# Kernel tuning notes

Measured on AMD Instinct MI355X. Metric: run time of the kernel, lower is better.

The kernel has to match this reference:

```python
import jax, jax.numpy as jnp
import numpy as np

D, H, COND, MLP_RATIO = 1024, 16, 1024, 4
HD = D // H
DFF = MLP_RATIO * D


def layer_norm(x, w, eps=1e-5):
    xf = x.astype(jnp.float32)
    mu = jnp.mean(xf, axis=-1, keepdims=True)
    var = jnp.mean((xf - mu) ** 2, axis=-1, keepdims=True)
    return (xf - mu) * jax.lax.rsqrt(var + eps) * w


def rms_norm(x, w, eps=1e-6):
    xf = x.astype(jnp.float32)
    rms = jnp.sqrt(jnp.mean(xf * xf, axis=-1, keepdims=True) + eps)
    return (xf / rms * w).astype(x.dtype)


def rotate_half(x):
    x1, x2 = x[..., : x.shape[-1] // 2], x[..., x.shape[-1] // 2:]
    return jnp.concatenate([-x2, x1], axis=-1)


def apply_rope(x, cos, sin):
    return x * cos + rotate_half(x) * sin


def setup_inputs() -> dict:
    key = jax.random.key(0)
    ks = jax.random.split(key, 16)
    B, S = 4, 2048
    pos = jnp.arange(S, dtype=jnp.float32)
    inv = 1.0 / (10000.0 ** (jnp.arange(0, HD, 2, dtype=jnp.float32) / HD))
    freqs = pos[:, None] * inv[None, :]              # (S, HD/2)
    emb = jnp.concatenate([freqs, freqs], axis=-1)   # (S, HD)
    return {
        "x": jax.random.normal(ks[0], (B, S, D), jnp.float32),
        "cos": jnp.cos(emb)[None, :, None, :],        # (1,S,1,HD)
        "sin": jnp.sin(emb)[None, :, None, :],
        "c": jax.random.normal(ks[1], (B, COND), jnp.float32),
        "norm1_w": jnp.ones((D,), jnp.float32),
        "Wqkv": jax.random.normal(ks[2], (D, 3 * D), jnp.float32) * 0.02,
        "Wout": jax.random.normal(ks[3], (D, D), jnp.float32) * 0.02,
        "q_norm_w": jnp.ones((HD,), jnp.float32),
        "k_norm_w": jnp.ones((HD,), jnp.float32),
        "norm2_w": jnp.ones((D,), jnp.float32),
        "W1": jax.random.normal(ks[4], (D, DFF), jnp.float32) * 0.02,
        "b1": jnp.zeros((DFF,), jnp.float32),
        "W2": jax.random.normal(ks[5], (DFF, D), jnp.float32) * 0.02,
        "b2": jnp.zeros((D,), jnp.float32),
        "ada_W": jax.random.normal(ks[6], (COND, 6 * D), jnp.float32) * 0.02,
        "ada_b": jnp.zeros((6 * D,), jnp.float32),
    }


def reference(x, cos, sin, c, norm1_w, Wqkv, Wout, q_norm_w, k_norm_w,
              norm2_w, W1, b1, W2, b2, ada_W, ada_b):
    B, S, _ = x.shape
    mod = (c @ ada_W + ada_b)[:, None, :]            # (B,1,6D)
    sh_msa, sc_msa, g_msa, sh_mlp, sc_mlp, g_mlp = jnp.split(mod, 6, axis=-1)

    x_norm = layer_norm(x, norm1_w) * (1 + sc_msa) + sh_msa
    qkv = (x_norm @ Wqkv).reshape(B, S, 3, H, HD)
    q, k, v = qkv[:, :, 0], qkv[:, :, 1], qkv[:, :, 2]  # (B,S,H,HD)
    q = apply_rope(rms_norm(q, q_norm_w), cos, sin)
    k = apply_rope(rms_norm(k, k_norm_w), cos, sin)

    scale = 1.0 / jnp.sqrt(jnp.float32(HD))
    logits = jnp.einsum('bqhd,bkhd->bhqk', q, k) * scale
    probs = jax.nn.softmax(logits, axis=-1)
    attn = jnp.einsum('bhqk,bkhd->bqhd', probs, v).reshape(B, S, D)

    x = x + g_msa * (attn @ Wout)

    x_norm = layer_norm(x, norm2_w) * (1 + sc_mlp) + sh_mlp
    h = jax.nn.gelu(x_norm @ W1 + b1, approximate=True)
    x = x + g_mlp * (h @ W2 + b2)
    return x
```

## Files before the change

kernel.cpp:

```cpp
#include <hip/hip_runtime.h>
#include <hip/hip_bf16.h>
#include <math.h>

typedef __bf16 bf16;
typedef __bf16 bf16x8 __attribute__((ext_vector_type(8)));
typedef __bf16 bf16x4 __attribute__((ext_vector_type(4)));
typedef float f32x4 __attribute__((ext_vector_type(4)));

#define S_LEN 2048
#define NTOK 8192
#define DIM 1024
#define NH 16
#define HEADD 64
#define DFF 4096
#define MODD 6144

__device__ __forceinline__ void gload_lds16(const bf16* g, bf16* l) {
  __builtin_amdgcn_global_load_lds(
      (const __attribute__((address_space(1))) void*)g,
      (__attribute__((address_space(3))) void*)l, 16, 0, 0);
}

__device__ __forceinline__ float gelu_tanh(float x) {
  float inner = 0.7978845608028654f * (x + 0.044715f * x * x * x);
  return 0.5f * x * (1.0f + tanhf(inner));
}

__global__ __launch_bounds__(256) void init_mod_kernel(
    const float* __restrict__ ada_b, float* __restrict__ mod) {
  int i = blockIdx.x * 256 + threadIdx.x;
  mod[i] = ada_b[i % MODD];
}

__global__ __launch_bounds__(256) void ada_gemm_kernel(
    const float* __restrict__ cnd, const float* __restrict__ W,
    float* __restrict__ mod) {
  int n = blockIdx.x * 256 + threadIdx.x;
  int k0 = blockIdx.y * 128;
  float a0 = 0.f, a1 = 0.f, a2 = 0.f, a3 = 0.f;
  for (int k = k0; k < k0 + 128; ++k) {
    float w = W[(size_t)k * MODD + n];
    a0 = fmaf(cnd[k], w, a0);
    a1 = fmaf(cnd[1024 + k], w, a1);
    a2 = fmaf(cnd[2048 + k], w, a2);
    a3 = fmaf(cnd[3072 + k], w, a3);
  }
  atomicAdd(&mod[n], a0);
  atomicAdd(&mod[MODD + n], a1);
  atomicAdd(&mod[2 * MODD + n], a2);
  atomicAdd(&mod[3 * MODD + n], a3);
}

__global__ __launch_bounds__(256) void transpose_cast_kernel(
    const float* __restrict__ W, bf16* __restrict__ Wt, int K, int N) {
  __shared__ float tile[32][33];
  int n0 = blockIdx.x * 32, k0 = blockIdx.y * 32;
  int r = threadIdx.x >> 3;
  int c4 = (threadIdx.x & 7) * 4;
  float4 v = *(const float4*)&W[(size_t)(k0 + r) * N + n0 + c4];
  tile[r][c4 + 0] = v.x; tile[r][c4 + 1] = v.y;
  tile[r][c4 + 2] = v.z; tile[r][c4 + 3] = v.w;
  __syncthreads();
  bf16x4 o;
  o[0] = (bf16)tile[c4 + 0][r];
  o[1] = (bf16)tile[c4 + 1][r];
  o[2] = (bf16)tile[c4 + 2][r];
  o[3] = (bf16)tile[c4 + 3][r];
  *(bf16x4*)&Wt[(size_t)(n0 + r) * K + k0 + c4] = o;
}

__global__ __launch_bounds__(256) void vtrans_kernel(
    const bf16* __restrict__ qkv, bf16* __restrict__ VT) {
  __shared__ __align__(16) bf16 t[64][72];
  const int bh = blockIdx.y;
  const int b = bh >> 4, h = bh & 15;
  const int s0 = blockIdx.x * 64;
  const int tid = threadIdx.x;
  {
    const int r = tid >> 2;
    const int c = (tid & 3) * 16;
    const bf16* src =
        qkv + (size_t)(b * S_LEN + s0 + r) * 3072 + 2048 + h * 64 + c;
    *(bf16x8*)&t[r][c] = *(const bf16x8*)src;
    *(bf16x8*)&t[r][c + 8] = *(const bf16x8*)(src + 8);
  }
  __syncthreads();
  {
    const int d = tid & 63;
    const int sc = (tid >> 6) * 16;
    bf16x8 o0, o1;
#pragma unroll
    for (int j = 0; j < 8; ++j) o0[j] = t[sc + j][d];
#pragma unroll
    for (int j = 0; j < 8; ++j) o1[j] = t[sc + 8 + j][d];
    bf16* dst = VT + (size_t)(bh * 64 + d) * S_LEN + s0 + sc;
    *(bf16x8*)dst = o0;
    *(bf16x8*)(dst + 8) = o1;
  }
}

__global__ __launch_bounds__(256) void ln_mod_kernel(
    const float* __restrict__ x, const float* __restrict__ w,
    const float* __restrict__ mod, int sh_off, int sc_off,
    bf16* __restrict__ out) {
  __shared__ float red[8];
  const int row = blockIdx.x;
  const int b = row >> 11;
  const int tid = threadIdx.x;
  const float4 v = ((const float4*)(x + (size_t)row * DIM))[tid];
  float s1 = v.x + v.y + v.z + v.w;
  float s2 = v.x * v.x + v.y * v.y + v.z * v.z + v.w * v.w;
  for (int off = 32; off > 0; off >>= 1) {
    s1 += __shfl_down(s1, off, 64);
    s2 += __shfl_down(s2, off, 64);
  }
  const int wid = tid >> 6;
  if ((tid & 63) == 0) { red[wid] = s1; red[4 + wid] = s2; }
  __syncthreads();
  s1 = red[0] + red[1] + red[2] + red[3];
  s2 = red[4] + red[5] + red[6] + red[7];
  const float mu = s1 * (1.0f / DIM);
  const float inv = rsqrtf(s2 * (1.0f / DIM) - mu * mu + 1e-5f);
  const int c = tid * 4;
  const float* mb = mod + (size_t)b * MODD;
  float xs[4] = {v.x, v.y, v.z, v.w};
  bf16x4 o;
#pragma unroll
  for (int j = 0; j < 4; ++j)
    o[j] = (bf16)(((xs[j] - mu) * inv) * w[c + j] * (1.0f + mb[sc_off + c + j]) +
                  mb[sh_off + c + j]);
  *(bf16x4*)(out + (size_t)row * DIM + c) = o;
}

template <int EPI>
__global__ __launch_bounds__(256) void gemm_bt(
    const bf16* __restrict__ A, const bf16* __restrict__ Bt,
    bf16* __restrict__ Cb, float* __restrict__ Cf,
    const float* __restrict__ bias, const float* __restrict__ gmod,
    const float* __restrict__ resid, int M, int N, int K) {
  __shared__ __align__(16) bf16 As[2][128 * 32];
  __shared__ __align__(16) bf16 Bs[2][128 * 32];
  const int tid = threadIdx.x;
  const int wid = tid >> 6;
  const int lane = tid & 63;
  const int l15 = lane & 15;
  const int quad = lane >> 4;
  const int m0 = blockIdx.y * 128;
  const int n0 = blockIdx.x * 128;
  const int wm = (wid & 1) * 64;
  const int wn = (wid >> 1) * 64;

  const int r0 = tid >> 2;
  const int cc0 = (tid & 3) * 8;
  const size_t a_base = (size_t)(m0 + r0) * K + cc0;
  const size_t a_base2 = (size_t)(m0 + 64 + r0) * K + cc0;
  const size_t b_base = (size_t)(n0 + r0) * K + cc0;
  const size_t b_base2 = (size_t)(n0 + 64 + r0) * K + cc0;

  f32x4 acc[4][4] = {};

  for (int kt = 0; kt < K; kt += 64) {
    gload_lds16(A + a_base + kt, &As[0][tid * 8]);
    gload_lds16(A + a_base2 + kt, &As[0][(256 + tid) * 8]);
    gload_lds16(Bt + b_base + kt, &Bs[0][tid * 8]);
    gload_lds16(Bt + b_base2 + kt, &Bs[0][(256 + tid) * 8]);
    gload_lds16(A + a_base + kt + 32, &As[1][tid * 8]);
    gload_lds16(A + a_base2 + kt + 32, &As[1][(256 + tid) * 8]);
    gload_lds16(Bt + b_base + kt + 32, &Bs[1][tid * 8]);
    gload_lds16(Bt + b_base2 + kt + 32, &Bs[1][(256 + tid) * 8]);
    __syncthreads();
#pragma unroll
    for (int half = 0; half < 2; ++half) {
      bf16x8 af[4], bfr[4];
#pragma unroll
      for (int i = 0; i < 4; ++i) {
        af[i] = *(const bf16x8*)&As[half][(wm + i * 16 + l15) * 32 + quad * 8];
        bfr[i] = *(const bf16x8*)&Bs[half][(wn + i * 16 + l15) * 32 + quad * 8];
      }
#pragma unroll
      for (int i = 0; i < 4; ++i)
#pragma unroll
        for (int j = 0; j < 4; ++j)
          acc[i][j] = __builtin_amdgcn_mfma_f32_16x16x32_bf16(af[i], bfr[j],
                                                              acc[i][j], 0, 0, 0);
    }
    __syncthreads();
  }

#pragma unroll
  for (int i = 0; i < 4; ++i) {
#pragma unroll
    for (int r = 0; r < 4; ++r) {
      const int m = m0 + wm + i * 16 + quad * 4 + r;
#pragma unroll
      for (int j = 0; j < 4; ++j) {
        const int n = n0 + wn + j * 16 + l15;
        float v = acc[i][j][r];
        if (EPI == 0) {
          Cb[(size_t)m * N + n] = (bf16)v;
        } else if (EPI == 1) {
          const int b = m >> 11;
          Cf[(size_t)m * N + n] =
              resid[(size_t)m * N + n] + gmod[(size_t)b * MODD + n] * v;
        } else if (EPI == 2) {
          v += bias[n];
          Cb[(size_t)m * N + n] = (bf16)gelu_tanh(v);
        } else {
          v += bias[n];
          const int b = m >> 11;
          Cf[(size_t)m * N + n] =
              resid[(size_t)m * N + n] + gmod[(size_t)b * MODD + n] * v;
        }
      }
    }
  }
}

__global__ __launch_bounds__(256) void rope_kernel(
    bf16* __restrict__ qkv, const float* __restrict__ cosb,
    const float* __restrict__ sinb, const float* __restrict__ qw,
    const float* __restrict__ kw) {
  const int wid = threadIdx.x >> 6;
  const int lane = threadIdx.x & 63;
  const int inst = blockIdx.x * 4 + wid;
  const int h = inst & (NH - 1);
  const int token = inst >> 4;
  const int s = token & (S_LEN - 1);
  const size_t base = (size_t)token * (3 * DIM) + h * HEADD + lane;
  const float cv = cosb[s * HEADD + lane];
  const float sv = sinb[s * HEADD + lane];
  const float sign = (lane < 32) ? -1.0f : 1.0f;
  {
    float xq = (float)qkv[base];
    float ss = xq * xq;
    for (int off = 1; off < 64; off <<= 1) ss += __shfl_xor(ss, off, 64);
    float rn = rsqrtf(ss * (1.0f / HEADD) + 1e-6f);
    float xn = xq * rn * qw[lane];
    float other = __shfl_xor(xn, 32, 64);
    qkv[base] = (bf16)(xn * cv + sign * other * sv);
  }
  {
    float xk = (float)qkv[base + DIM];
    float ss = xk * xk;
    for (int off = 1; off < 64; off <<= 1) ss += __shfl_xor(ss, off, 64);
    float rn = rsqrtf(ss * (1.0f / HEADD) + 1e-6f);
    float xn = xk * rn * kw[lane];
    float other = __shfl_xor(xn, 32, 64);
    qkv[base + DIM] = (bf16)(xn * cv + sign * other * sv);
  }
}

__global__ __launch_bounds__(256) void attn_kernel(
    const bf16* __restrict__ qkv, const bf16* __restrict__ VT,
    bf16* __restrict__ out) {
  __shared__ __align__(16) bf16 Ks[64][72];
  __shared__ __align__(16) bf16 Vs[64][72];
  __shared__ __align__(16) bf16 Ps[4][32][72];
  const int bh = blockIdx.y;
  const int b = bh >> 4;
  const int h = bh & 15;
  const int q0 = blockIdx.x * 128;
  const int tid = threadIdx.x;
  const int wid = tid >> 6;
  const int lane = tid & 63;
  const int l15 = lane & 15;
  const int quad = lane >> 4;

  bf16x8 aq[2][2];
#pragma unroll
  for (int i = 0; i < 2; ++i) {
    const int qrow = q0 + wid * 32 + i * 16 + l15;
    const size_t qbase = (size_t)(b * S_LEN + qrow) * (3 * DIM) + h * HEADD;
    aq[i][0] = *(const bf16x8*)(qkv + qbase + quad * 8);
    aq[i][1] = *(const bf16x8*)(qkv + qbase + 32 + quad * 8);
  }

  const int sr = tid >> 3;
  const int sc8 = (tid & 7) * 8;
  const float cexp = 0.125f * 1.44269504f;

  f32x4 oacc[2][4] = {};
  float psum[2][4] = {{0.f, 0.f, 0.f, 0.f}, {0.f, 0.f, 0.f, 0.f}};

  for (int kt = 0; kt < S_LEN; kt += 64) {
    __syncthreads();
#pragma unroll
    for (int rep = 0; rep < 2; ++rep) {
      const int r = rep * 32 + sr;
      *(bf16x8*)&Ks[r][sc8] = *(const bf16x8*)(
          qkv + (size_t)(b * S_LEN + kt + r) * (3 * DIM) + DIM + h * HEADD + sc8);
      *(bf16x8*)&Vs[r][sc8] = *(const bf16x8*)(
          VT + (size_t)(bh * 64 + r) * S_LEN + kt + sc8);
    }
    __syncthreads();

    f32x4 sc[2][4] = {};
#pragma unroll
    for (int cc = 0; cc < 4; ++cc) {
      const bf16x8 b0 = *(const bf16x8*)&Ks[cc * 16 + l15][quad * 8];
      const bf16x8 b1 = *(const bf16x8*)&Ks[cc * 16 + l15][32 + quad * 8];
#pragma unroll
      for (int i = 0; i < 2; ++i) {
        sc[i][cc] = __builtin_amdgcn_mfma_f32_16x16x32_bf16(aq[i][0], b0, sc[i][cc], 0, 0, 0);
        sc[i][cc] = __builtin_amdgcn_mfma_f32_16x16x32_bf16(aq[i][1], b1, sc[i][cc], 0, 0, 0);
      }
    }

#pragma unroll
    for (int i = 0; i < 2; ++i)
#pragma unroll
      for (int cc = 0; cc < 4; ++cc)
#pragma unroll
        for (int r = 0; r < 4; ++r) {
          const float p = __builtin_amdgcn_exp2f(fmaf(sc[i][cc][r], cexp, -8.0f));
          psum[i][r] += p;
          Ps[wid][i * 16 + quad * 4 + r][cc * 16 + l15] = (bf16)p;
        }

    bf16x8 pa[2][2];
#pragma unroll
    for (int i = 0; i < 2; ++i) {
      pa[i][0] = *(const bf16x8*)&Ps[wid][i * 16 + l15][quad * 8];
      pa[i][1] = *(const bf16x8*)&Ps[wid][i * 16 + l15][32 + quad * 8];
    }
#pragma unroll
    for (int j = 0; j < 4; ++j) {
      const bf16x8 v0 = *(const bf16x8*)&Vs[j * 16 + l15][quad * 8];
      const bf16x8 v1 = *(const bf16x8*)&Vs[j * 16 + l15][32 + quad * 8];
#pragma unroll
      for (int i = 0; i < 2; ++i) {
        oacc[i][j] = __builtin_amdgcn_mfma_f32_16x16x32_bf16(pa[i][0], v0, oacc[i][j], 0, 0, 0);
        oacc[i][j] = __builtin_amdgcn_mfma_f32_16x16x32_bf16(pa[i][1], v1, oacc[i][j], 0, 0, 0);
      }
    }
  }

#pragma unroll
  for (int i = 0; i < 2; ++i)
#pragma unroll
    for (int r = 0; r < 4; ++r) {
      float ps = psum[i][r];
#pragma unroll
      for (int off = 1; off < 16; off <<= 1) ps += __shfl_xor(ps, off, 64);
      const int m = q0 + wid * 32 + i * 16 + quad * 4 + r;
      const float invl = 1.0f / ps;
#pragma unroll
      for (int j = 0; j < 4; ++j)
        out[((size_t)(b * S_LEN + m) * NH + h) * HEADD + j * 16 + l15] =
            (bf16)(oacc[i][j][r] * invl);
    }
}

extern "C" void kernel_launch(void* const* d_in, const int* in_sizes, int n_in,
                              void* d_out, int out_size, void* d_ws,
                              size_t ws_size, hipStream_t stream) {
  const float* x = (const float*)d_in[0];
  const float* cosb = (const float*)d_in[1];
  const float* sinb = (const float*)d_in[2];
  const float* cnd = (const float*)d_in[3];
  const float* norm1_w = (const float*)d_in[4];
  const float* Wqkv = (const float*)d_in[5];
  const float* Wout = (const float*)d_in[6];
  const float* q_norm_w = (const float*)d_in[7];
  const float* k_norm_w = (const float*)d_in[8];
  const float* norm2_w = (const float*)d_in[9];
  const float* W1 = (const float*)d_in[10];
  const float* b1 = (const float*)d_in[11];
  const float* W2 = (const float*)d_in[12];
  const float* b2 = (const float*)d_in[13];
  const float* ada_W = (const float*)d_in[14];
  const float* ada_b = (const float*)d_in[15];
  float* out = (float*)d_out;

  char* p = (char*)d_ws;
  float* mod = (float*)p;   p += (size_t)4 * MODD * 4;
  bf16* WqkvT = (bf16*)p;   p += (size_t)3072 * 1024 * 2;
  bf16* WoutT = (bf16*)p;   p += (size_t)1024 * 1024 * 2;
  bf16* W1T = (bf16*)p;     p += (size_t)4096 * 1024 * 2;
  bf16* W2T = (bf16*)p;     p += (size_t)1024 * 4096 * 2;
  bf16* XN = (bf16*)p;      p += (size_t)NTOK * DIM * 2;
  bf16* QKV = (bf16*)p;     p += (size_t)NTOK * 3 * DIM * 2;
  bf16* ATTN = (bf16*)p;    p += (size_t)NTOK * DIM * 2;
  bf16* Hbuf = (bf16*)p;    p += (size_t)NTOK * DFF * 2;
  bf16* VT = Hbuf;

  init_mod_kernel<<<96, 256, 0, stream>>>(ada_b, mod);
  ada_gemm_kernel<<<dim3(24, 8), 256, 0, stream>>>(cnd, ada_W, mod);
  transpose_cast_kernel<<<dim3(96, 32), 256, 0, stream>>>(Wqkv, WqkvT, 1024, 3072);
  transpose_cast_kernel<<<dim3(32, 32), 256, 0, stream>>>(Wout, WoutT, 1024, 1024);
  transpose_cast_kernel<<<dim3(128, 32), 256, 0, stream>>>(W1, W1T, 1024, 4096);
  transpose_cast_kernel<<<dim3(32, 128), 256, 0, stream>>>(W2, W2T, 4096, 1024);
  ln_mod_kernel<<<NTOK, 256, 0, stream>>>(x, norm1_w, mod, 0, 1024, XN);
  gemm_bt<0><<<dim3(24, 64), 256, 0, stream>>>(XN, WqkvT, QKV, nullptr, nullptr,
                                               nullptr, nullptr, NTOK, 3072, 1024);
  rope_kernel<<<NTOK * NH / 4, 256, 0, stream>>>(QKV, cosb, sinb, q_norm_w, k_norm_w);
  vtrans_kernel<<<dim3(32, 64), 256, 0, stream>>>(QKV, VT);
  attn_kernel<<<dim3(16, 64), 256, 0, stream>>>(QKV, VT, ATTN);
  gemm_bt<1><<<dim3(8, 64), 256, 0, stream>>>(ATTN, WoutT, nullptr, out, nullptr,
                                              mod + 2 * 1024, x, NTOK, 1024, 1024);
  ln_mod_kernel<<<NTOK, 256, 0, stream>>>(out, norm2_w, mod, 3 * 1024, 4 * 1024, XN);
  gemm_bt<2><<<dim3(32, 64), 256, 0, stream>>>(XN, W1T, Hbuf, nullptr, b1, nullptr,
                                               nullptr, NTOK, DFF, 1024);
  gemm_bt<3><<<dim3(8, 64), 256, 0, stream>>>(Hbuf, W2T, nullptr, out, b2,
                                              mod + 5 * 1024, out, NTOK, 1024, DFF);
  (void)in_sizes; (void)n_in; (void)out_size; (void)ws_size;
}
```

Measured before the change: 684.2 us.

## Keep attention probabilities in registers via transposed QK^T and swizzled LDS

The attention kernel now computes S^T by swapping the MFMA operands (K as A, Q as B). Each lane's score outputs then line up with the B-operand layout of a 16x16x16 bf16 MFMA for the PV product, so probabilities feed straight from registers and the Ps shared-memory round trip and its bank traffic go away. K and V tiles use an XOR-swizzled unpadded LDS layout to avoid bank conflicts, and the row-sum reduction is reorganized to fit the transposed layout. The cost is twice as many PV MFMA instructions at half the K depth, plus more intricate indexing that must stay consistent.

```diff
diff --git a/kernel.cpp b/kernel.cpp
--- a/kernel.cpp
+++ b/kernel.cpp
@@ -6,6 +6,7 @@
 typedef __bf16 bf16x8 __attribute__((ext_vector_type(8)));
 typedef __bf16 bf16x4 __attribute__((ext_vector_type(4)));
 typedef float f32x4 __attribute__((ext_vector_type(4)));
+typedef short s16x4 __attribute__((ext_vector_type(4)));
 
 #define S_LEN 2048
 #define NTOK 8192
@@ -253,9 +254,8 @@
 __global__ __launch_bounds__(256) void attn_kernel(
     const bf16* __restrict__ qkv, const bf16* __restrict__ VT,
     bf16* __restrict__ out) {
-  __shared__ __align__(16) bf16 Ks[64][72];
-  __shared__ __align__(16) bf16 Vs[64][72];
-  __shared__ __align__(16) bf16 Ps[4][32][72];
+  __shared__ __align__(16) bf16 Ks[4096];
+  __shared__ __align__(16) bf16 Vs[4096];
   const int bh = blockIdx.y;
   const int b = bh >> 4;
   const int h = bh & 15;
@@ -275,80 +275,88 @@
     aq[i][1] = *(const bf16x8*)(qkv + qbase + 32 + quad * 8);
   }
 
-  const int sr = tid >> 3;
-  const int sc8 = (tid & 7) * 8;
+  const int rstage = tid & 63;
+  const int kbase = tid >> 6;
   const float cexp = 0.125f * 1.44269504f;
 
   f32x4 oacc[2][4] = {};
-  float psum[2][4] = {{0.f, 0.f, 0.f, 0.f}, {0.f, 0.f, 0.f, 0.f}};
+  float psum[2] = {0.f, 0.f};
 
   for (int kt = 0; kt < S_LEN; kt += 64) {
     __syncthreads();
-#pragma unroll
-    for (int rep = 0; rep < 2; ++rep) {
-      const int r = rep * 32 + sr;
-      *(bf16x8*)&Ks[r][sc8] = *(const bf16x8*)(
-          qkv + (size_t)(b * S_LEN + kt + r) * (3 * DIM) + DIM + h * HEADD + sc8);
-      *(bf16x8*)&Vs[r][sc8] = *(const bf16x8*)(
-          VT + (size_t)(bh * 64 + r) * S_LEN + kt + sc8);
+    const bf16* krow = qkv + (size_t)(b * S_LEN + kt + rstage) * 3072 + DIM + h * HEADD;
+    const bf16* vrow = VT + (size_t)(bh * 64 + rstage) * S_LEN + kt;
+    const int rsw = rstage & 7;
+#pragma unroll
+    for (int rr = 0; rr < 2; ++rr) {
+      const int ck = kbase + 4 * rr;
+      const int sw = ((ck ^ rsw) << 3);
+      *(bf16x8*)&Ks[rstage * 64 + sw] = *(const bf16x8*)(krow + ck * 8);
+      *(bf16x8*)&Vs[rstage * 64 + sw] = *(const bf16x8*)(vrow + ck * 8);
     }
     __syncthreads();
 
     f32x4 sc[2][4] = {};
 #pragma unroll
-    for (int cc = 0; cc < 4; ++cc) {
-      const bf16x8 b0 = *(const bf16x8*)&Ks[cc * 16 + l15][quad * 8];
-      const bf16x8 b1 = *(const bf16x8*)&Ks[cc * 16 + l15][32 + quad * 8];
-#pragma unroll
-      for (int i = 0; i < 2; ++i) {
-        sc[i][cc] = __builtin_amdgcn_mfma_f32_16x16x32_bf16(aq[i][0], b0, sc[i][cc], 0, 0, 0);
-        sc[i][cc] = __builtin_amdgcn_mfma_f32_16x16x32_bf16(aq[i][1], b1, sc[i][cc], 0, 0, 0);
+    for (int hh = 0; hh < 2; ++hh) {
+#pragma unroll
+      for (int cc = 0; cc < 4; ++cc) {
+        const int row = cc * 16 + l15;
+        const bf16x8 kf = *(const bf16x8*)&Ks[row * 64 + (((quad + 4 * hh) ^ (l15 & 7)) << 3)];
+#pragma unroll
+        for (int i = 0; i < 2; ++i)
+          sc[i][cc] = __builtin_amdgcn_mfma_f32_16x16x32_bf16(kf, aq[i][hh],
+                                                              sc[i][cc], 0, 0, 0);
       }
     }
 
+    s16x4 pf[2][4];
 #pragma unroll
     for (int i = 0; i < 2; ++i)
 #pragma unroll
-      for (int cc = 0; cc < 4; ++cc)
+      for (int cc = 0; cc < 4; ++cc) {
+        bf16x4 pb;
 #pragma unroll
         for (int r = 0; r < 4; ++r) {
           const float p = __builtin_amdgcn_exp2f(fmaf(sc[i][cc][r], cexp, -8.0f));
-          psum[i][r] += p;
-          Ps[wid][i * 16 + quad * 4 + r][cc * 16 + l15] = (bf16)p;
+          psum[i] += p;
+          pb[r] = (bf16)p;
         }
-
-    bf16x8 pa[2][2];
-#pragma unroll
-    for (int i = 0; i < 2; ++i) {
-      pa[i][0] = *(const bf16x8*)&Ps[wid][i * 16 + l15][quad * 8];
-      pa[i][1] = *(const bf16x8*)&Ps[wid][i * 16 + l15][32 + quad * 8];
-    }
+        pf[i][cc] = __builtin_bit_cast(s16x4, pb);
+      }
+
 #pragma unroll
     for (int j = 0; j < 4; ++j) {
-      const bf16x8 v0 = *(const bf16x8*)&Vs[j * 16 + l15][quad * 8];
-      const bf16x8 v1 = *(const bf16x8*)&Vs[j * 16 + l15][32 + quad * 8];
-#pragma unroll
-      for (int i = 0; i < 2; ++i) {
-        oacc[i][j] = __builtin_amdgcn_mfma_f32_16x16x32_bf16(pa[i][0], v0, oacc[i][j], 0, 0, 0);
-        oacc[i][j] = __builtin_amdgcn_mfma_f32_16x16x32_bf16(pa[i][1], v1, oacc[i][j], 0, 0, 0);
+      const int d = 16 * j + l15;
+      const int drow = d * 64;
+      const int dsw = d & 7;
+#pragma unroll
+      for (int cc = 0; cc < 4; ++cc) {
+        const int ck = 2 * cc + (quad >> 1);
+        const s16x4 vf = *(const s16x4*)&Vs[drow + ((ck ^ dsw) << 3) + ((quad & 1) << 2)];
+#pragma unroll
+        for (int i = 0; i < 2; ++i)
+          oacc[i][j] = __builtin_amdgcn_mfma_f32_16x16x16bf16_1k(pf[i][cc], vf,
+                                                                 oacc[i][j], 0, 0, 0);
       }
     }
   }
 
 #pragma unroll
-  for (int i = 0; i < 2; ++i)
+  for (int i = 0; i < 2; ++i) {
+    float ps = psum[i];
+    ps += __shfl_xor(ps, 16, 64);
+    ps += __shfl_xor(ps, 32, 64);
 #pragma unroll
     for (int r = 0; r < 4; ++r) {
-      float ps = psum[i][r];
-#pragma unroll
-      for (int off = 1; off < 16; off <<= 1) ps += __shfl_xor(ps, off, 64);
+      const float invl = 1.0f / __shfl(ps, quad * 4 + r, 64);
       const int m = q0 + wid * 32 + i * 16 + quad * 4 + r;
-      const float invl = 1.0f / ps;
 #pragma unroll
       for (int j = 0; j < 4; ++j)
         out[((size_t)(b * S_LEN + m) * NH + h) * HEADD + j * 16 + l15] =
             (bf16)(oacc[i][j][r] * invl);
     }
+  }
 }
 
 extern "C" void kernel_launch(void* const* d_in, const int* in_sizes, int n_in,
```

After: 681.4 us. About the same (-0.4%).
